# Kernel tuning notes

Measured on AMD Instinct MI355X. Metric: run time of the kernel, lower is better.

The kernel has to match this reference:

```python
import jax, jax.numpy as jnp
import numpy as np

HIDDEN = 256
N_HEADS = 8
HEAD_DIM = HIDDEN // N_HEADS
SCALE = HEAD_DIM ** -0.5
LN_EPS = 1e-5


def entmax15(z):
    """Entmax-1.5 along the last axis (Peters et al. 2019 exact algorithm)."""
    z = z / 2.0
    z = z - jnp.max(z, axis=-1, keepdims=True)
    zs = jnp.flip(jnp.sort(z, axis=-1), axis=-1)          # descending
    K = z.shape[-1]
    k = jnp.arange(1, K + 1, dtype=z.dtype)
    mean = jnp.cumsum(zs, axis=-1) / k
    mean_sq = jnp.cumsum(zs * zs, axis=-1) / k
    ss = k * (mean_sq - mean * mean)
    delta = (1.0 - ss) / k
    tau = mean - jnp.sqrt(jnp.maximum(delta, 1e-12))
    support = (tau <= zs).astype(jnp.int32)
    k_star = jnp.sum(support, axis=-1, keepdims=True)      # support size >=1
    tau_star = jnp.take_along_axis(tau, k_star - 1, axis=-1)
    p = jnp.square(jnp.maximum(z - tau_star, 0.0))
    return p


def _attend(q, kv, W_q, W_k, W_v, log_temp):
    B, K, H = kv.shape
    qh = (q @ W_q.T).reshape(B, N_HEADS, HEAD_DIM)                 # (B,n,d)
    kh = (kv @ W_k.T).reshape(B, K, N_HEADS, HEAD_DIM)             # (B,K,n,d)
    vh = (kv @ W_v.T).reshape(B, K, N_HEADS, HEAD_DIM)
    scores = jnp.einsum('bnd,bknd->bnk', qh, kh) * (SCALE * jnp.exp(log_temp))
    attn = entmax15(scores)                                        # (B,n,K) sparse
    ctx = jnp.einsum('bnk,bknd->bnd', attn, vh).reshape(B, H)
    return ctx


def layernorm(x, gamma, beta):
    mu = jnp.mean(x, axis=-1, keepdims=True)
    var = jnp.mean(jnp.square(x - mu), axis=-1, keepdims=True)
    return (x - mu) * jax.lax.rsqrt(var + LN_EPS) * gamma + beta


def setup_inputs() -> dict:
    key = jax.random.key(0)
    ks = jax.random.split(key, 12)
    B, K, H = 32, 8192, HIDDEN
    s = 0.02
    return {
        'z_gene': jax.random.normal(ks[0], (B, H), jnp.float32),
        'z_cpg_seq': jax.random.normal(ks[1], (B, K, H), jnp.float32),
        'z_mirna_seq': jax.random.normal(ks[2], (B, K, H), jnp.float32),
        'W_q': jax.random.normal(ks[3], (H, H), jnp.float32) * s,
        'W_k_cpg': jax.random.normal(ks[4], (H, H), jnp.float32) * s,
        'W_v_cpg': jax.random.normal(ks[5], (H, H), jnp.float32) * s,
        'W_k_mirna': jax.random.normal(ks[6], (H, H), jnp.float32) * s,
        'W_v_mirna': jax.random.normal(ks[7], (H, H), jnp.float32) * s,
        'W_out': jax.random.normal(ks[8], (H, 2 * H), jnp.float32) * s,
        'b_out': jnp.zeros((H,), jnp.float32),
        'ln_gamma': jnp.ones((H,), jnp.float32),
        'ln_beta': jnp.zeros((H,), jnp.float32),
        'modality_logits': jnp.zeros((2,), jnp.float32),
        'log_temp': jnp.zeros((), jnp.float32),
    }


def reference(z_gene, z_cpg_seq, z_mirna_seq, W_q, W_k_cpg, W_v_cpg,
              W_k_mirna, W_v_mirna, W_out, b_out, ln_gamma, ln_beta,
              modality_logits, log_temp):
    ctx_cpg = _attend(z_gene, z_cpg_seq, W_q, W_k_cpg, W_v_cpg, log_temp)
    ctx_mirna = _attend(z_gene, z_mirna_seq, W_q, W_k_mirna, W_v_mirna, log_temp)
    w = jax.nn.softmax(modality_logits)
    combined = jnp.concatenate([w[0] * ctx_cpg, w[1] * ctx_mirna], axis=-1)
    fused = layernorm(combined @ W_out.T + b_out + z_gene, ln_gamma, ln_beta)
    return fused
```

## Files before the change

kernel.cpp:

```cpp
#include <hip/hip_runtime.h>
#include <hip/hip_bf16.h>
#include <cstdint>
#include <cstddef>

#define HIDDEN 256
#define NHEADS 8
#define HDIM 32
#define KLEN 8192
#define BATCH 32
#define NSPLIT 16
#define LN_EPS 1e-5f

typedef __attribute__((ext_vector_type(8))) short bf16x8;
typedef __attribute__((ext_vector_type(4))) float f32x4;

#define OFF_QT    ((size_t)0)
#define SZ_QT     ((size_t)2*BATCH*NHEADS*HIDDEN)
#define OFF_SC    (OFF_QT + SZ_QT)
#define SZ_SC     ((size_t)2*BATCH*KLEN*NHEADS)
#define OFF_UP    (OFF_SC + SZ_SC)
#define SZ_UP     ((size_t)2*BATCH*NSPLIT*NHEADS*HIDDEN)
#define OFF_COMB  (OFF_UP + SZ_UP)
#define SZ_COMB   ((size_t)BATCH*2*HIDDEN)

static __device__ inline short f2b(float f) {
    __hip_bfloat16 h = __float2bfloat16(f);
    return (short)__builtin_bit_cast(unsigned short, h);
}

__global__ void k_prep(const float* __restrict__ zg, const float* __restrict__ Wq,
                       const float* __restrict__ Wk0, const float* __restrict__ Wk1,
                       const float* __restrict__ log_temp, float* __restrict__ qt) {
    int b = blockIdx.x, t = threadIdx.x;
    __shared__ float z[HIDDEN];
    __shared__ float qh[HIDDEN];
    z[t] = zg[(size_t)b*HIDDEN + t];
    __syncthreads();
    const float4* wr4 = (const float4*)(Wq + (size_t)t*HIDDEN);
    const float4* z4 = (const float4*)z;
    float acc = 0.f;
    #pragma unroll 8
    for (int i = 0; i < HIDDEN/4; ++i) {
        float4 w = wr4[i], zz = z4[i];
        acc += w.x*zz.x + w.y*zz.y + w.z*zz.z + w.w*zz.w;
    }
    qh[t] = acc;
    __syncthreads();
    float alpha = 0.5f * rsqrtf((float)HDIM) * __expf(log_temp[0]);
    for (int m = 0; m < 2; ++m) {
        const float* Wk = m ? Wk1 : Wk0;
        for (int n = 0; n < NHEADS; ++n) {
            float a = 0.f;
            #pragma unroll 8
            for (int d = 0; d < HDIM; ++d) {
                a += qh[n*HDIM + d] * Wk[(size_t)(n*HDIM + d)*HIDDEN + t];
            }
            qt[(((size_t)m*BATCH + b)*NHEADS + n)*HIDDEN + t] = a * alpha;
        }
    }
}

__global__ void __launch_bounds__(256, 3) k_scores(const float* __restrict__ kv0,
                                                   const float* __restrict__ kv1,
                                                   const float* __restrict__ qt,
                                                   float* __restrict__ sc) {
    int bid = blockIdx.x;
    int slab = bid & 31;
    int mb = bid >> 5;
    int t = threadIdx.x;
    int wave = t >> 6, l = t & 63;
    int row16 = l & 15, kgrp = l >> 4;
    const float* kv = ((mb >> 5) ? kv1 : kv0) + (size_t)(mb & 31)*KLEN*HIDDEN;

    const float* qb = qt + (size_t)mb*NHEADS*HIDDEN + (size_t)((l & 15) & 7)*HIDDEN + kgrp*8;
    bf16x8 fq[8];
    #pragma unroll
    for (int c = 0; c < 8; ++c) {
        float4 qa = *(const float4*)(qb + c*32);
        float4 qc = *(const float4*)(qb + c*32 + 4);
        bf16x8 q;
        q[0] = f2b(qa.x); q[1] = f2b(qa.y); q[2] = f2b(qa.z); q[3] = f2b(qa.w);
        q[4] = f2b(qc.x); q[5] = f2b(qc.y); q[6] = f2b(qc.z); q[7] = f2b(qc.w);
        fq[c] = q;
    }
    float* out = sc + (size_t)mb*KLEN*NHEADS;
    int rbase = slab*256 + wave*64;

    for (int tt = 0; tt < 4; ++tt) {
        int R = rbase + tt*16;
        const float* ptr = kv + (size_t)(R + row16)*HIDDEN + kgrp*8;
        float4 va[8], vb[8];
        #pragma unroll
        for (int c = 0; c < 8; ++c) {
            va[c] = *(const float4*)(ptr + c*32);
            vb[c] = *(const float4*)(ptr + c*32 + 4);
        }
        f32x4 acc = {0.f, 0.f, 0.f, 0.f};
        #pragma unroll
        for (int c = 0; c < 8; ++c) {
            bf16x8 a;
            a[0] = f2b(va[c].x); a[1] = f2b(va[c].y); a[2] = f2b(va[c].z); a[3] = f2b(va[c].w);
            a[4] = f2b(vb[c].x); a[5] = f2b(vb[c].y); a[6] = f2b(vb[c].z); a[7] = f2b(vb[c].w);
            acc = __builtin_amdgcn_mfma_f32_16x16x32_bf16(a, fq[c], acc, 0, 0, 0);
        }
        if ((l & 15) < 8) {
            int col = l & 15;
            #pragma unroll
            for (int r = 0; r < 4; ++r) {
                out[(size_t)(R + kgrp*4 + r)*NHEADS + col] = acc[r];
            }
        }
    }
}

__global__ void __launch_bounds__(256) k_entmax(float* __restrict__ sc) {
    int bid = blockIdx.x;
    int n = bid & 7, b = (bid >> 3) & 31, m = bid >> 8;
    int t = threadIdx.x;
    __shared__ float zs[KLEN];
    __shared__ float red[4];
    float* src = sc + ((size_t)m*BATCH + b)*KLEN*NHEADS + n;
    float mx = -1e30f;
    #pragma unroll
    for (int i = 0; i < KLEN/256; ++i) {
        float v = src[(size_t)(t + i*256)*NHEADS];
        zs[t + i*256] = v;
        mx = fmaxf(mx, v);
    }
    for (int off = 32; off; off >>= 1) mx = fmaxf(mx, __shfl_xor(mx, off));
    if ((t & 63) == 0) red[t >> 6] = mx;
    __syncthreads();
    mx = fmaxf(fmaxf(red[0], red[1]), fmaxf(red[2], red[3]));
    __syncthreads();
    const float4* z4 = (const float4*)zs;
    float lo = mx - 1.0f, hi = mx;
    for (int it = 0; it < 26; ++it) {
        float tm = 0.5f*(lo + hi);
        float s = 0.f;
        #pragma unroll
        for (int i = 0; i < 8; ++i) {
            float4 zz = z4[t + i*256];
            float d;
            d = fmaxf(zz.x - tm, 0.f); s = fmaf(d, d, s);
            d = fmaxf(zz.y - tm, 0.f); s = fmaf(d, d, s);
            d = fmaxf(zz.z - tm, 0.f); s = fmaf(d, d, s);
            d = fmaxf(zz.w - tm, 0.f); s = fmaf(d, d, s);
        }
        for (int off = 32; off; off >>= 1) s += __shfl_xor(s, off);
        if ((t & 63) == 0) red[t >> 6] = s;
        __syncthreads();
        s = red[0] + red[1] + red[2] + red[3];
        __syncthreads();
        if (s >= 1.0f) lo = tm; else hi = tm;
    }
    float tfin = 0.5f*(lo + hi);
    #pragma unroll
    for (int i = 0; i < KLEN/256; ++i) {
        float d = fmaxf(zs[t + i*256] - tfin, 0.f);
        src[(size_t)(t + i*256)*NHEADS] = d*d;
    }
}

__global__ void __launch_bounds__(256, 3) k_ctxsum(const float* __restrict__ kv0,
                                                   const float* __restrict__ kv1,
                                                   const float* __restrict__ sc,
                                                   float* __restrict__ upart) {
    int rb = (int)gridDim.x - 1 - (int)blockIdx.x;
    int s = rb & (NSPLIT - 1);
    int mb = rb / NSPLIT;
    int t = threadIdx.x;
    int wave = t >> 6, l = t & 63;
    int col16 = l & 15, kgrp = l >> 4;
    int hn = col16 & 7;
    const float* kv = ((mb >> 5) ? kv1 : kv0) + (size_t)(mb & 31)*KLEN*HIDDEN;
    const float* pbase = sc + (size_t)mb*KLEN*NHEADS;

    f32x4 accs[16];
    #pragma unroll
    for (int ct = 0; ct < 16; ++ct) accs[ct] = (f32x4){0.f, 0.f, 0.f, 0.f};

    int kbase = s*512 + wave*128;
    for (int kc = 0; kc < 4; ++kc) {
        int k0 = kbase + kc*32 + kgrp*8;
        float pf[8];
        #pragma unroll
        for (int j = 0; j < 8; ++j) pf[j] = pbase[(size_t)(k0 + j)*NHEADS + hn];
        bf16x8 afrag;
        afrag[0] = f2b(pf[0]); afrag[1] = f2b(pf[1]); afrag[2] = f2b(pf[2]); afrag[3] = f2b(pf[3]);
        afrag[4] = f2b(pf[4]); afrag[5] = f2b(pf[5]); afrag[6] = f2b(pf[6]); afrag[7] = f2b(pf[7]);
        const float* brow = kv + (size_t)k0*HIDDEN + col16;
        #pragma unroll
        for (int ct = 0; ct < 16; ++ct) {
            float bf[8];
            #pragma unroll
            for (int j = 0; j < 8; ++j) bf[j] = brow[(size_t)j*HIDDEN + ct*16];
            bf16x8 bfrag;
            bfrag[0] = f2b(bf[0]); bfrag[1] = f2b(bf[1]); bfrag[2] = f2b(bf[2]); bfrag[3] = f2b(bf[3]);
            bfrag[4] = f2b(bf[4]); bfrag[5] = f2b(bf[5]); bfrag[6] = f2b(bf[6]); bfrag[7] = f2b(bf[7]);
            accs[ct] = __builtin_amdgcn_mfma_f32_16x16x32_bf16(afrag, bfrag, accs[ct], 0, 0, 0);
        }
    }
    __shared__ float redls[4*NHEADS*HIDDEN];
    if (kgrp < 2) {
        #pragma unroll
        for (int ct = 0; ct < 16; ++ct) {
            #pragma unroll
            for (int r = 0; r < 4; ++r) {
                int row = kgrp*4 + r;
                redls[((size_t)wave*NHEADS + row)*HIDDEN + ct*16 + col16] = accs[ct][r];
            }
        }
    }
    __syncthreads();
    float* up = upart + ((size_t)mb*NSPLIT + s)*NHEADS*HIDDEN;
    float4* red4 = (float4*)redls;
    int n = t >> 5, hq = (t & 31)*2;
    #pragma unroll
    for (int j = 0; j < 2; ++j) {
        float4 sum = red4[((size_t)0*NHEADS + n)*64 + hq + j];
        #pragma unroll
        for (int w = 1; w < 4; ++w) {
            float4 v = red4[((size_t)w*NHEADS + n)*64 + hq + j];
            sum.x += v.x; sum.y += v.y; sum.z += v.z; sum.w += v.w;
        }
        ((float4*)(up + (size_t)n*HIDDEN))[hq + j] = sum;
    }
}

__global__ void k_ctx(const float* __restrict__ upart, const float* __restrict__ Wv0,
                      const float* __restrict__ Wv1, const float* __restrict__ mlogits,
                      float* __restrict__ comb) {
    int b = blockIdx.x, t = threadIdx.x;
    __shared__ float ul[NHEADS*260];
    float l0 = mlogits[0], l1 = mlogits[1];
    float mxl = fmaxf(l0, l1);
    float e0 = __expf(l0 - mxl), e1 = __expf(l1 - mxl);
    float w0 = e0/(e0 + e1), w1 = e1/(e0 + e1);
    for (int m = 0; m < 2; ++m) {
        const float* Wv = m ? Wv1 : Wv0;
        float wm = m ? w1 : w0;
        __syncthreads();
        for (int n = 0; n < NHEADS; ++n) {
            float s = 0.f;
            const float* up = upart + ((size_t)m*BATCH + b)*NSPLIT*NHEADS*HIDDEN
                              + (size_t)n*HIDDEN + t;
            #pragma unroll
            for (int c = 0; c < NSPLIT; ++c) s += up[(size_t)c*NHEADS*HIDDEN];
            ul[n*260 + t] = s;
        }
        __syncthreads();
        int n = t >> 5;
        const float4* wr4 = (const float4*)(Wv + (size_t)t*HIDDEN);
        const float4* uu4 = (const float4*)(ul + n*260);
        float acc = 0.f;
        #pragma unroll 8
        for (int i = 0; i < HIDDEN/4; ++i) {
            float4 w = wr4[i], uu = uu4[i];
            acc += w.x*uu.x + w.y*uu.y + w.z*uu.z + w.w*uu.w;
        }
        comb[(size_t)b*(2*HIDDEN) + (size_t)m*HIDDEN + t] = acc * wm;
    }
}

__global__ void k_out(const float* __restrict__ comb, const float* __restrict__ Wout,
                      const float* __restrict__ bout, const float* __restrict__ zg,
                      const float* __restrict__ gamma, const float* __restrict__ beta,
                      float* __restrict__ out) {
    int b = blockIdx.x, t = threadIdx.x;
    __shared__ float cl[2*HIDDEN];
    __shared__ float red[4];
    cl[t] = comb[(size_t)b*512 + t];
    cl[t + 256] = comb[(size_t)b*512 + 256 + t];
    __syncthreads();
    float acc = bout[t] + zg[(size_t)b*HIDDEN + t];
    const float4* wr4 = (const float4*)(Wout + (size_t)t*512);
    const float4* cl4 = (const float4*)cl;
    #pragma unroll 8
    for (int i = 0; i < 512/4; ++i) {
        float4 w = wr4[i], c = cl4[i];
        acc += w.x*c.x + w.y*c.y + w.z*c.z + w.w*c.w;
    }
    float s = acc;
    for (int off = 32; off; off >>= 1) s += __shfl_xor(s, off);
    if ((t & 63) == 0) red[t >> 6] = s;
    __syncthreads();
    float mu = (red[0] + red[1] + red[2] + red[3]) * (1.0f/HIDDEN);
    __syncthreads();
    float dv = acc - mu;
    float vs = dv*dv;
    for (int off = 32; off; off >>= 1) vs += __shfl_xor(vs, off);
    if ((t & 63) == 0) red[t >> 6] = vs;
    __syncthreads();
    float var = (red[0] + red[1] + red[2] + red[3]) * (1.0f/HIDDEN);
    out[(size_t)b*HIDDEN + t] = dv * rsqrtf(var + LN_EPS) * gamma[t] + beta[t];
}

extern "C" void kernel_launch(void* const* d_in, const int* in_sizes, int n_in,
                              void* d_out, int out_size, void* d_ws, size_t ws_size,
                              hipStream_t stream) {
    const float* zg    = (const float*)d_in[0];
    const float* cpg   = (const float*)d_in[1];
    const float* mir   = (const float*)d_in[2];
    const float* Wq    = (const float*)d_in[3];
    const float* Wk0   = (const float*)d_in[4];
    const float* Wv0   = (const float*)d_in[5];
    const float* Wk1   = (const float*)d_in[6];
    const float* Wv1   = (const float*)d_in[7];
    const float* Wout  = (const float*)d_in[8];
    const float* bout  = (const float*)d_in[9];
    const float* gam   = (const float*)d_in[10];
    const float* bet   = (const float*)d_in[11];
    const float* mlog  = (const float*)d_in[12];
    const float* ltemp = (const float*)d_in[13];

    float* ws    = (float*)d_ws;
    float* qt    = ws + OFF_QT;
    float* sc    = ws + OFF_SC;
    float* up    = ws + OFF_UP;
    float* comb  = ws + OFF_COMB;
    float* out   = (float*)d_out;

    hipLaunchKernelGGL(k_prep,    dim3(BATCH),            dim3(256), 0, stream,
                       zg, Wq, Wk0, Wk1, ltemp, qt);
    hipLaunchKernelGGL(k_scores,  dim3(2*BATCH*32),       dim3(256), 0, stream,
                       cpg, mir, qt, sc);
    hipLaunchKernelGGL(k_entmax,  dim3(2*BATCH*NHEADS),   dim3(256), 0, stream,
                       sc);
    hipLaunchKernelGGL(k_ctxsum,  dim3(2*BATCH*NSPLIT),   dim3(256), 0, stream,
                       cpg, mir, sc, up);
    hipLaunchKernelGGL(k_ctx,     dim3(BATCH),            dim3(256), 0, stream,
                       up, Wv0, Wv1, mlog, comb);
    hipLaunchKernelGGL(k_out,     dim3(BATCH),            dim3(256), 0, stream,
                       comb, Wout, bout, zg, gam, bet, out);
}
```

Measured before the change: 349.5 us.

## Cache bf16 copy of KV in scores pass and reuse it for context sum

```diff
diff --git a/kernel.cpp b/kernel.cpp
--- a/kernel.cpp
+++ b/kernel.cpp
@@ -18,14 +18,23 @@
 #define SZ_QT     ((size_t)2*BATCH*NHEADS*HIDDEN)
 #define OFF_SC    (OFF_QT + SZ_QT)
 #define SZ_SC     ((size_t)2*BATCH*KLEN*NHEADS)
-#define OFF_UP    (OFF_SC + SZ_SC)
+#define OFF_PT    (OFF_SC + SZ_SC)
+#define SZ_PT     ((size_t)2*BATCH*KLEN*NHEADS)
+#define OFF_UP    (OFF_PT + SZ_PT)
 #define SZ_UP     ((size_t)2*BATCH*NSPLIT*NHEADS*HIDDEN)
 #define OFF_COMB  (OFF_UP + SZ_UP)
 #define SZ_COMB   ((size_t)BATCH*2*HIDDEN)
+#define OFF_KVB_BYTES ((OFF_COMB + SZ_COMB) * 4)
+#define SZ_KVB_BYTES  ((size_t)2*BATCH*KLEN*HIDDEN*2)
+#define WS_NEEDED     (OFF_KVB_BYTES + SZ_KVB_BYTES)
 
 static __device__ inline short f2b(float f) {
     __hip_bfloat16 h = __float2bfloat16(f);
     return (short)__builtin_bit_cast(unsigned short, h);
+}
+static __device__ inline float b2f(short s) {
+    unsigned u = ((unsigned)(unsigned short)s) << 16;
+    return __builtin_bit_cast(float, u);
 }
 
 __global__ void k_prep(const float* __restrict__ zg, const float* __restrict__ Wq,
@@ -63,7 +72,9 @@
 __global__ void __launch_bounds__(256, 3) k_scores(const float* __restrict__ kv0,
                                                    const float* __restrict__ kv1,
                                                    const float* __restrict__ qt,
-                                                   float* __restrict__ sc) {
+                                                   float* __restrict__ sc,
+                                                   unsigned short* __restrict__ kvb,
+                                                   int do_cache) {
     int bid = blockIdx.x;
     int slab = bid & 31;
     int mb = bid >> 5;
@@ -71,6 +82,7 @@
     int wave = t >> 6, l = t & 63;
     int row16 = l & 15, kgrp = l >> 4;
     const float* kv = ((mb >> 5) ? kv1 : kv0) + (size_t)(mb & 31)*KLEN*HIDDEN;
+    unsigned short* kvbm = kvb + (size_t)mb*KLEN*HIDDEN;
 
     const float* qb = qt + (size_t)mb*NHEADS*HIDDEN + (size_t)((l & 15) & 7)*HIDDEN + kgrp*8;
     bf16x8 fq[8];
@@ -101,6 +113,9 @@
             bf16x8 a;
             a[0] = f2b(va[c].x); a[1] = f2b(va[c].y); a[2] = f2b(va[c].z); a[3] = f2b(va[c].w);
             a[4] = f2b(vb[c].x); a[5] = f2b(vb[c].y); a[6] = f2b(vb[c].z); a[7] = f2b(vb[c].w);
+            if (do_cache) {
+                *(bf16x8*)(kvbm + (size_t)(R + row16)*HIDDEN + c*32 + kgrp*8) = a;
+            }
             acc = __builtin_amdgcn_mfma_f32_16x16x32_bf16(a, fq[c], acc, 0, 0, 0);
         }
         if ((l & 15) < 8) {
@@ -113,13 +128,15 @@
     }
 }
 
-__global__ void __launch_bounds__(256) k_entmax(float* __restrict__ sc) {
+__global__ void __launch_bounds__(256) k_entmax(float* __restrict__ sc,
+                                                float* __restrict__ pT) {
     int bid = blockIdx.x;
     int n = bid & 7, b = (bid >> 3) & 31, m = bid >> 8;
+    int mb = m*BATCH + b;
     int t = threadIdx.x;
     __shared__ float zs[KLEN];
     __shared__ float red[4];
-    float* src = sc + ((size_t)m*BATCH + b)*KLEN*NHEADS + n;
+    float* src = sc + (size_t)mb*KLEN*NHEADS + n;
     float mx = -1e30f;
     #pragma unroll
     for (int i = 0; i < KLEN/256; ++i) {
@@ -154,17 +171,82 @@
         if (s >= 1.0f) lo = tm; else hi = tm;
     }
     float tfin = 0.5f*(lo + hi);
+    float* pTn = pT + ((size_t)mb*NHEADS + n)*KLEN;
     #pragma unroll
     for (int i = 0; i < KLEN/256; ++i) {
         float d = fmaxf(zs[t + i*256] - tfin, 0.f);
-        src[(size_t)(t + i*256)*NHEADS] = d*d;
-    }
-}
-
-__global__ void __launch_bounds__(256, 3) k_ctxsum(const float* __restrict__ kv0,
-                                                   const float* __restrict__ kv1,
-                                                   const float* __restrict__ sc,
-                                                   float* __restrict__ upart) {
+        float p = d*d;
+        src[(size_t)(t + i*256)*NHEADS] = p;
+        pTn[t + i*256] = p;
+    }
+}
+
+__global__ void __launch_bounds__(256, 4) k_ctxsum_bf(const unsigned short* __restrict__ kvb,
+                                                      const float* __restrict__ pT,
+                                                      float* __restrict__ upart) {
+    int rb = (int)gridDim.x - 1 - (int)blockIdx.x;
+    int s = rb & (NSPLIT - 1);
+    int mb = rb / NSPLIT;
+    int t = threadIdx.x;
+    int wave = t >> 6, l = t & 63;
+    int half = l >> 5, hseg = l & 31;
+    const unsigned short* kvm = kvb + (size_t)mb*KLEN*HIDDEN;
+    const float* pTm = pT + (size_t)mb*NHEADS*KLEN;
+
+    float acc[8][8];
+    #pragma unroll
+    for (int n = 0; n < 8; ++n)
+        #pragma unroll
+        for (int j = 0; j < 8; ++j) acc[n][j] = 0.f;
+
+    int kbase = s*512 + wave*128;
+    for (int it = 0; it < 64; ++it) {
+        int k = kbase + it*2 + half;
+        bf16x8 kvv = *(const bf16x8*)(kvm + (size_t)k*HIDDEN + hseg*8);
+        float kf[8];
+        #pragma unroll
+        for (int j = 0; j < 8; ++j) kf[j] = b2f(kvv[j]);
+        #pragma unroll
+        for (int n = 0; n < 8; ++n) {
+            float p = pTm[(size_t)n*KLEN + k];
+            acc[n][0] = fmaf(p, kf[0], acc[n][0]);
+            acc[n][1] = fmaf(p, kf[1], acc[n][1]);
+            acc[n][2] = fmaf(p, kf[2], acc[n][2]);
+            acc[n][3] = fmaf(p, kf[3], acc[n][3]);
+            acc[n][4] = fmaf(p, kf[4], acc[n][4]);
+            acc[n][5] = fmaf(p, kf[5], acc[n][5]);
+            acc[n][6] = fmaf(p, kf[6], acc[n][6]);
+            acc[n][7] = fmaf(p, kf[7], acc[n][7]);
+        }
+    }
+    #pragma unroll
+    for (int n = 0; n < 8; ++n)
+        #pragma unroll
+        for (int j = 0; j < 8; ++j)
+            acc[n][j] += __shfl_xor(acc[n][j], 32);
+    __shared__ float lds[4][NHEADS][HIDDEN];
+    if (half == 0) {
+        #pragma unroll
+        for (int n = 0; n < 8; ++n)
+            #pragma unroll
+            for (int j = 0; j < 8; ++j)
+                lds[wave][n][hseg*8 + j] = acc[n][j];
+    }
+    __syncthreads();
+    float* up = upart + ((size_t)mb*NSPLIT + s)*NHEADS*HIDDEN;
+    #pragma unroll
+    for (int q = 0; q < 8; ++q) {
+        int pid = q*256 + t;
+        int n = pid >> 8, h = pid & 255;
+        float ssum = lds[0][n][h] + lds[1][n][h] + lds[2][n][h] + lds[3][n][h];
+        up[(size_t)n*HIDDEN + h] = ssum;
+    }
+}
+
+__global__ void __launch_bounds__(256, 3) k_ctxsum_f32(const float* __restrict__ kv0,
+                                                       const float* __restrict__ kv1,
+                                                       const float* __restrict__ sc,
+                                                       float* __restrict__ upart) {
     int rb = (int)gridDim.x - 1 - (int)blockIdx.x;
     int s = rb & (NSPLIT - 1);
     int mb = rb / NSPLIT;
@@ -316,18 +398,27 @@
     float* ws    = (float*)d_ws;
     float* qt    = ws + OFF_QT;
     float* sc    = ws + OFF_SC;
+    float* pT    = ws + OFF_PT;
     float* up    = ws + OFF_UP;
     float* comb  = ws + OFF_COMB;
+    unsigned short* kvb = (unsigned short*)((char*)d_ws + OFF_KVB_BYTES);
     float* out   = (float*)d_out;
+
+    int do_cache = (ws_size >= (size_t)WS_NEEDED) ? 1 : 0;
 
     hipLaunchKernelGGL(k_prep,    dim3(BATCH),            dim3(256), 0, stream,
                        zg, Wq, Wk0, Wk1, ltemp, qt);
     hipLaunchKernelGGL(k_scores,  dim3(2*BATCH*32),       dim3(256), 0, stream,
-                       cpg, mir, qt, sc);
+                       cpg, mir, qt, sc, kvb, do_cache);
     hipLaunchKernelGGL(k_entmax,  dim3(2*BATCH*NHEADS),   dim3(256), 0, stream,
-                       sc);
-    hipLaunchKernelGGL(k_ctxsum,  dim3(2*BATCH*NSPLIT),   dim3(256), 0, stream,
-                       cpg, mir, sc, up);
+                       sc, pT);
+    if (do_cache) {
+        hipLaunchKernelGGL(k_ctxsum_bf, dim3(2*BATCH*NSPLIT), dim3(256), 0, stream,
+                           kvb, pT, up);
+    } else {
+        hipLaunchKernelGGL(k_ctxsum_f32, dim3(2*BATCH*NSPLIT), dim3(256), 0, stream,
+                           cpg, mir, sc, up);
+    }
     hipLaunchKernelGGL(k_ctx,     dim3(BATCH),            dim3(256), 0, stream,
                        up, Wv0, Wv1, mlog, comb);
     hipLaunchKernelGGL(k_out,     dim3(BATCH),            dim3(256), 0, stream,
```

Measured after the change: 373.9 us. 1.07x slower.
